# Kernel tuning notes

Hardware: AMD Instinct MI355X
Metric: run time of the kernel (lower is better)

Reference implementation:

```python
import jax, jax.numpy as jnp
import numpy as np

N = 50000   # nodes
E = 800000  # edges (before self-loops)


def _gcn_conv(X, W, b, src, dst, dinv, n):
    # PyG GCNConv: out[i] = sum_j norm_ij * (X W)[j] + b, norm_ij = d_i^-1/2 d_j^-1/2
    h = X @ W                                   # [N, d_out]
    norm = dinv[src] * dinv[dst]                # [E+N]
    msg = h[src] * norm[:, None]                # gather + scale
    return jax.ops.segment_sum(msg, dst, num_segments=n) + b


def setup_inputs() -> dict:
    key = jax.random.key(0)
    k1, k2, k3, k4 = jax.random.split(key, 4)
    X = jax.random.normal(k1, (N, 128), dtype=jnp.float32)
    edge_index = jax.random.randint(k2, (2, E), 0, N, dtype=jnp.int64)
    W1 = jax.random.normal(k3, (128, 128), dtype=jnp.float32) * (1.0 / np.sqrt(128))
    b1 = jnp.zeros((128,), jnp.float32)
    W2 = jax.random.normal(k4, (128, 64), dtype=jnp.float32) * (1.0 / np.sqrt(128))
    b2 = jnp.zeros((64,), jnp.float32)
    return {"X": X, "edge_index": edge_index, "W1": W1, "b1": b1, "W2": W2, "b2": b2}


def reference(X, edge_index, W1, b1, W2, b2):
    n = X.shape[0]
    loops = jnp.arange(n, dtype=edge_index.dtype)
    src = jnp.concatenate([edge_index[0], loops])   # A + I
    dst = jnp.concatenate([edge_index[1], loops])
    deg = jax.ops.segment_sum(jnp.ones(src.shape[0], X.dtype), dst, num_segments=n)
    dinv = jnp.where(deg > 0, jax.lax.rsqrt(deg), 0.0)

    h = _gcn_conv(X, W1, b1, src, dst, dinv, n)                     # gcn1
    h = jax.nn.relu(_gcn_conv(h, W1, b1, src, dst, dinv, n))        # gcn1 again (as in source), relu
    # dropout: eval mode (identity)
    logits = _gcn_conv(h, W2, b2, src, dst, dinv, n)                # gcn2
    return jax.nn.log_softmax(logits, axis=1)
```

## Files before the change

kernel.cpp:

```cpp
#include <hip/hip_runtime.h>
#include <hip/hip_fp16.h>
#include <type_traits>

typedef _Float16 f16x8 __attribute__((ext_vector_type(8)));
typedef float    f32x4 __attribute__((ext_vector_type(4)));

__device__ inline unsigned int pack2(float a, float b) {
    __half2 h = __floats2half2_rn(a, b);
    return *(unsigned int*)&h;
}
__device__ inline float2 unpack2(unsigned int u) {
    __half2 h = *(__half2*)&u;
    return __half22float2(h);
}

#define MAXB 8192


__global__ void zero_kernel(int* __restrict__ p, int len) {
    int i = blockIdx.x * blockDim.x + threadIdx.x;
    if (i < len) p[i] = 0;
}

__global__ __launch_bounds__(256) void bucket_scatter_kernel(
    const int* __restrict__ src, const int* __restrict__ dst, int E, int nbuck,
    int* __restrict__ bcursor, unsigned int* __restrict__ staging) {
    __shared__ int hist[256];
    __shared__ int base[256];
    const int t = threadIdx.x;
    const int chunk = (E + gridDim.x - 1) / gridDim.x;
    const int e0 = blockIdx.x * chunk;
    const int e1 = min(E, e0 + chunk);
    for (int i = t; i < nbuck; i += 256) hist[i] = 0;
    __syncthreads();
    for (int e = e0 + t; e < e1; e += 256)
        atomicAdd(&hist[((unsigned)dst[e]) >> 8], 1);
    __syncthreads();
    for (int i = t; i < nbuck; i += 256) {
        int c = hist[i];
        base[i] = (c > 0) ? atomicAdd(&bcursor[i], c) : 0;
        hist[i] = 0;
    }
    __syncthreads();
    for (int e = e0 + t; e < e1; e += 256) {
        int d = dst[e];
        int b = ((unsigned)d) >> 8;
        int off = atomicAdd(&hist[b], 1);
        staging[(size_t)b * MAXB + base[b] + off] =
            (unsigned)src[e] | ((unsigned)(d & 255) << 16);
    }
}

__global__ __launch_bounds__(256) void bucket_hist_kernel(
    const unsigned int* __restrict__ staging, const int* __restrict__ bcursor,
    int n, int* __restrict__ counts, float* __restrict__ dinv) {
    __shared__ int hist[256];
    const int b = blockIdx.x, t = threadIdx.x;
    hist[t] = 0;
    __syncthreads();
    const int cnt = bcursor[b];
    const unsigned int* rec = staging + (size_t)b * MAXB;
    for (int i = t; i < cnt; i += 256) atomicAdd(&hist[(rec[i] >> 16) & 255], 1);
    __syncthreads();
    int node = (b << 8) + t;
    if (node < n) {
        int c = hist[t];
        counts[node] = c;
        dinv[node]   = rsqrtf(1.0f + (float)c);
    }
}

__global__ __launch_bounds__(256) void scan_small_kernel(const int* __restrict__ in,
                                                         int* __restrict__ out, int nb) {
    __shared__ int s[256];
    int t = threadIdx.x;
    int v = (t < nb) ? in[t] : 0;
    s[t] = v;
    __syncthreads();
    for (int off = 1; off < 256; off <<= 1) {
        int u = (t >= off) ? s[t - off] : 0;
        __syncthreads();
        s[t] += u;
        __syncthreads();
    }
    if (t < nb) out[t] = s[t] - v;
}

__global__ __launch_bounds__(256) void scan_write_kernel(const int* __restrict__ counts,
                                                         const int* __restrict__ blockoff, int n,
                                                         int* __restrict__ rowptr) {
    __shared__ int s[256];
    int t = threadIdx.x;
    int i = blockIdx.x * 256 + t;
    int v = (i < n) ? counts[i] : 0;
    s[t] = v;
    __syncthreads();
    for (int off = 1; off < 256; off <<= 1) {
        int u = (t >= off) ? s[t - off] : 0;
        __syncthreads();
        s[t] += u;
        __syncthreads();
    }
    int excl = blockoff[blockIdx.x] + s[t] - v;
    if (i < n) {
        rowptr[i] = excl;
        if (i == n - 1) rowptr[n] = excl + v;
    }
}

__global__ __launch_bounds__(256) void bucket_place_kernel(
    const unsigned int* __restrict__ staging, const int* __restrict__ bcursor,
    const int* __restrict__ rowptr, int n, unsigned short* __restrict__ edges) {
    __shared__ int lcur[256];
    const int b = blockIdx.x, t = threadIdx.x;
    int node = (b << 8) + t;
    lcur[t] = rowptr[min(node, n)];
    __syncthreads();
    const int cnt = bcursor[b];
    const unsigned int* rec = staging + (size_t)b * MAXB;
    for (int i = t; i < cnt; i += 256) {
        unsigned r = rec[i];
        int dl = (r >> 16) & 255;
        int p  = atomicAdd(&lcur[dl], 1);
        edges[p] = (unsigned short)(r & 0xffffu);
    }
}

template <int DOUT, typename TIN>
__global__ __launch_bounds__(256) void gemm_mfma(const TIN* __restrict__ A,
                                                 const float* __restrict__ W,
                                                 const float* __restrict__ dinv,
                                                 __half* __restrict__ C, int n) {
    constexpr int NF = DOUT / 16;
    __shared__ __align__(16) unsigned char wlds[DOUT * 256];

    const int t = threadIdx.x;
    for (int p = t; p < 64 * DOUT; p += 256) {
        int nn = p % DOUT;
        int k  = (p / DOUT) * 2;
        float w0 = W[(size_t)k * DOUT + nn];
        float w1 = W[(size_t)(k + 1) * DOUT + nn];
        int byte = (nn * 256 + k * 2) ^ ((nn & 7) << 4);
        *(unsigned int*)(wlds + byte) = pack2(w0, w1);
    }
    __syncthreads();

    const int w  = t >> 6;
    const int l  = t & 63;
    const int m  = (blockIdx.x * 4 + w) * 16 + (l & 15);
    const int kq = l >> 4;
    const bool valid = (m < n);

    f32x4 acc[NF];
#pragma unroll
    for (int i = 0; i < NF; ++i) acc[i] = (f32x4){0.f, 0.f, 0.f, 0.f};

#pragma unroll
    for (int ks = 0; ks < 4; ++ks) {
        const int k0 = ks * 32 + kq * 8;
        f16x8 af = {0, 0, 0, 0, 0, 0, 0, 0};
        if (valid) {
            if constexpr (std::is_same<TIN, float>::value) {
                const float4 x0 = *(const float4*)&A[(size_t)m * 128 + k0];
                const float4 x1 = *(const float4*)&A[(size_t)m * 128 + k0 + 4];
                af[0] = (_Float16)x0.x; af[1] = (_Float16)x0.y;
                af[2] = (_Float16)x0.z; af[3] = (_Float16)x0.w;
                af[4] = (_Float16)x1.x; af[5] = (_Float16)x1.y;
                af[6] = (_Float16)x1.z; af[7] = (_Float16)x1.w;
            } else {
                af = *(const f16x8*)&A[(size_t)m * 128 + k0];
            }
        }
#pragma unroll
        for (int nf = 0; nf < NF; ++nf) {
            int nn = nf * 16 + (l & 15);
            int byte = (nn * 256 + k0 * 2) ^ ((nn & 7) << 4);
            f16x8 bf = *(const f16x8*)(wlds + byte);
            acc[nf] = __builtin_amdgcn_mfma_f32_16x16x32_f16(bf, af, acc[nf], 0, 0, 0);
        }
    }

    if (valid) {
        const float di = dinv[m];
#pragma unroll
        for (int nf = 0; nf < NF; ++nf) {
            uint2 o;
            o.x = pack2(di * acc[nf][0], di * acc[nf][1]);
            o.y = pack2(di * acc[nf][2], di * acc[nf][3]);
            *(uint2*)&C[(size_t)m * DOUT + nf * 16 + kq * 4] = o;
        }
    }
}

template <int DOUT, bool RELU, bool LSM, typename TOUT>
__global__ __launch_bounds__(256) void agg_kernel(const __half* __restrict__ H,
                                                  const int* __restrict__ rowptr,
                                                  const unsigned short* __restrict__ edges,
                                                  const float* __restrict__ dinv,
                                                  const float* __restrict__ bias,
                                                  TOUT* __restrict__ out, int n) {
    constexpr int LPR = DOUT / 8;
    constexpr int RPB = 256 / LPR;
    const int row  = blockIdx.x * RPB + threadIdx.x / LPR;
    const int lane = threadIdx.x % LPR;
    if (row >= n) return;

    const uint4* Hv = (const uint4*)H;

    float a[8];
    {
        uint4 h = Hv[(size_t)row * LPR + lane];
        float2 f;
        f = unpack2(h.x); a[0] = f.x; a[1] = f.y;
        f = unpack2(h.y); a[2] = f.x; a[3] = f.y;
        f = unpack2(h.z); a[4] = f.x; a[5] = f.y;
        f = unpack2(h.w); a[6] = f.x; a[7] = f.y;
    }
    auto accum = [&](uint4 h) {
        float2 f;
        f = unpack2(h.x); a[0] += f.x; a[1] += f.y;
        f = unpack2(h.y); a[2] += f.x; a[3] += f.y;
        f = unpack2(h.z); a[4] += f.x; a[5] += f.y;
        f = unpack2(h.w); a[6] += f.x; a[7] += f.y;
    };

    int j        = rowptr[row];
    const int je = rowptr[row + 1];
    for (; j + 3 < je; j += 4) {
        int s0 = edges[j];
        int s1 = edges[j + 1];
        int s2 = edges[j + 2];
        int s3 = edges[j + 3];
        uint4 h0 = Hv[(size_t)s0 * LPR + lane];
        uint4 h1 = Hv[(size_t)s1 * LPR + lane];
        uint4 h2 = Hv[(size_t)s2 * LPR + lane];
        uint4 h3 = Hv[(size_t)s3 * LPR + lane];
        accum(h0); accum(h1); accum(h2); accum(h3);
    }
    for (; j < je; ++j) accum(Hv[(size_t)edges[j] * LPR + lane]);

    const float di = dinv[row];
    const float4 b0 = ((const float4*)bias)[lane * 2];
    const float4 b1 = ((const float4*)bias)[lane * 2 + 1];
    a[0] = b0.x + di * a[0]; a[1] = b0.y + di * a[1];
    a[2] = b0.z + di * a[2]; a[3] = b0.w + di * a[3];
    a[4] = b1.x + di * a[4]; a[5] = b1.y + di * a[5];
    a[6] = b1.z + di * a[6]; a[7] = b1.w + di * a[7];

    if (RELU) {
#pragma unroll
        for (int i = 0; i < 8; ++i) a[i] = fmaxf(a[i], 0.f);
    }

    if constexpr (LSM) {
        float m8 = a[0];
#pragma unroll
        for (int i = 1; i < 8; ++i) m8 = fmaxf(m8, a[i]);
#pragma unroll
        for (int off = 1; off < LPR; off <<= 1) m8 = fmaxf(m8, __shfl_xor(m8, off, LPR));
        float s = 0.f;
#pragma unroll
        for (int i = 0; i < 8; ++i) s += expf(a[i] - m8);
#pragma unroll
        for (int off = 1; off < LPR; off <<= 1) s += __shfl_xor(s, off, LPR);
        float ls = m8 + logf(s);
        float* op = (float*)out + (size_t)row * DOUT + lane * 8;
        *(float4*)op       = make_float4(a[0] - ls, a[1] - ls, a[2] - ls, a[3] - ls);
        *(float4*)(op + 4) = make_float4(a[4] - ls, a[5] - ls, a[6] - ls, a[7] - ls);
    } else {
        uint4 o;
        o.x = pack2(a[0], a[1]);
        o.y = pack2(a[2], a[3]);
        o.z = pack2(a[4], a[5]);
        o.w = pack2(a[6], a[7]);
        *(uint4*)&((__half*)out)[(size_t)row * DOUT + lane * 8] = o;
    }
}


extern "C" void kernel_launch(void* const* d_in, const int* in_sizes, int n_in,
                              void* d_out, int out_size, void* d_ws, size_t ws_size,
                              hipStream_t stream) {
    const float* X  = (const float*)d_in[0];
    const int*   ei = (const int*)d_in[1];
    const float* W1 = (const float*)d_in[2];
    const float* b1 = (const float*)d_in[3];
    const float* W2 = (const float*)d_in[4];
    const float* b2 = (const float*)d_in[5];

    const int n = in_sizes[0] / 128;
    const int E = in_sizes[1] / 2;
    const int* src = ei;
    const int* dst = ei + E;
    const int nbuck = (n + 255) >> 8;

    char* ws = (char*)d_ws;
    size_t off = 0;
    auto alloc = [&](size_t bytes) -> void* {
        void* p = ws + off;
        off = (off + bytes + 255) & ~(size_t)255;
        return p;
    };
    int*            bcursor = (int*)  alloc((size_t)nbuck * 4);
    float*          dinv    = (float*)alloc((size_t)n * 4);
    int*            counts  = (int*)  alloc((size_t)n * 4);
    int*            rowptr  = (int*)  alloc((size_t)(n + 1) * 4);
    int*            bexcl   = (int*)  alloc((size_t)nbuck * 4);
    unsigned int*   staging = (unsigned int*)alloc((size_t)nbuck * MAXB * 4);
    unsigned short* edges   = (unsigned short*)alloc((size_t)E * 2);
    __half*         P       = (__half*)alloc((size_t)n * 128 * 2);
    __half*         Q       = (__half*)alloc((size_t)n * 128 * 2);

    const int nb = (n + 255) / 256;

    zero_kernel<<<1, 256, 0, stream>>>(bcursor, nbuck);
    bucket_scatter_kernel<<<392, 256, 0, stream>>>(src, dst, E, nbuck, bcursor, staging);
    bucket_hist_kernel<<<nbuck, 256, 0, stream>>>(staging, bcursor, n, counts, dinv);
    scan_small_kernel<<<1, 256, 0, stream>>>(bcursor, bexcl, nbuck);
    scan_write_kernel<<<nb, 256, 0, stream>>>(counts, bexcl, n, rowptr);
    bucket_place_kernel<<<nbuck, 256, 0, stream>>>(staging, bcursor, rowptr, n, edges);

    const int gb   = (n + 63) / 64;
    const int ab16 = (n + 15) / 16;
    const int ab32 = (n + 31) / 32;

    gemm_mfma<128, float><<<gb, 256, 0, stream>>>(X, W1, dinv, P, n);
    agg_kernel<128, false, false, __half><<<ab16, 256, 0, stream>>>(
        P, rowptr, edges, dinv, b1, Q, n);

    gemm_mfma<128, __half><<<gb, 256, 0, stream>>>(Q, W1, dinv, P, n);
    agg_kernel<128, true, false, __half><<<ab16, 256, 0, stream>>>(
        P, rowptr, edges, dinv, b1, Q, n);

    gemm_mfma<64, __half><<<gb, 256, 0, stream>>>(Q, W2, dinv, P, n);
    agg_kernel<64, false, true, float><<<ab32, 256, 0, stream>>>(
        P, rowptr, edges, dinv, b2, (float*)d_out, n);
}
```

Measured before the change: 172.5 us.

## Shard 128-wide features into column slabs and pin aggregation slabs per XCC

```diff
diff --git a/kernel.cpp b/kernel.cpp
--- a/kernel.cpp
+++ b/kernel.cpp
@@ -70,11 +70,24 @@
     }
 }
 
-__global__ __launch_bounds__(256) void scan_small_kernel(const int* __restrict__ in,
-                                                         int* __restrict__ out, int nb) {
+__global__ __launch_bounds__(256) void scan_write_kernel(const int* __restrict__ counts,
+                                                         const int* __restrict__ bcursor,
+                                                         int nbuck, int n,
+                                                         int* __restrict__ rowptr) {
+    __shared__ int sb[256];
     __shared__ int s[256];
     int t = threadIdx.x;
-    int v = (t < nb) ? in[t] : 0;
+    sb[t] = (t < nbuck) ? bcursor[t] : 0;
+    __syncthreads();
+    for (int off = 1; off < 256; off <<= 1) {
+        int u = (t >= off) ? sb[t - off] : 0;
+        __syncthreads();
+        sb[t] += u;
+        __syncthreads();
+    }
+    const int blockoff = (blockIdx.x == 0) ? 0 : sb[blockIdx.x - 1];
+    int i = blockIdx.x * 256 + t;
+    int v = (i < n) ? counts[i] : 0;
     s[t] = v;
     __syncthreads();
     for (int off = 1; off < 256; off <<= 1) {
@@ -83,25 +96,7 @@
         s[t] += u;
         __syncthreads();
     }
-    if (t < nb) out[t] = s[t] - v;
-}
-
-__global__ __launch_bounds__(256) void scan_write_kernel(const int* __restrict__ counts,
-                                                         const int* __restrict__ blockoff, int n,
-                                                         int* __restrict__ rowptr) {
-    __shared__ int s[256];
-    int t = threadIdx.x;
-    int i = blockIdx.x * 256 + t;
-    int v = (i < n) ? counts[i] : 0;
-    s[t] = v;
-    __syncthreads();
-    for (int off = 1; off < 256; off <<= 1) {
-        int u = (t >= off) ? s[t - off] : 0;
-        __syncthreads();
-        s[t] += u;
-        __syncthreads();
-    }
-    int excl = blockoff[blockIdx.x] + s[t] - v;
+    int excl = blockoff + s[t] - v;
     if (i < n) {
         rowptr[i] = excl;
         if (i == n - 1) rowptr[n] = excl + v;
@@ -126,7 +121,7 @@
     }
 }
 
-template <int DOUT, typename TIN>
+template <int DOUT, typename TIN, bool OUTQ>
 __global__ __launch_bounds__(256) void gemm_mfma(const TIN* __restrict__ A,
                                                  const float* __restrict__ W,
                                                  const float* __restrict__ dinv,
@@ -168,7 +163,7 @@
                 af[4] = (_Float16)x1.x; af[5] = (_Float16)x1.y;
                 af[6] = (_Float16)x1.z; af[7] = (_Float16)x1.w;
             } else {
-                af = *(const f16x8*)&A[(size_t)m * 128 + k0];
+                af = *(const f16x8*)&A[((size_t)ks * n + m) * 32 + kq * 8];
             }
         }
 #pragma unroll
@@ -187,21 +182,109 @@
             uint2 o;
             o.x = pack2(di * acc[nf][0], di * acc[nf][1]);
             o.y = pack2(di * acc[nf][2], di * acc[nf][3]);
-            *(uint2*)&C[(size_t)m * DOUT + nf * 16 + kq * 4] = o;
+            if constexpr (OUTQ)
+                *(uint2*)&C[((size_t)(nf >> 1) * n + m) * 32 + (nf & 1) * 16 + kq * 4] = o;
+            else
+                *(uint2*)&C[(size_t)m * DOUT + nf * 16 + kq * 4] = o;
         }
     }
 }
 
-template <int DOUT, bool RELU, bool LSM, typename TOUT>
-__global__ __launch_bounds__(256) void agg_kernel(const __half* __restrict__ H,
-                                                  const int* __restrict__ rowptr,
-                                                  const unsigned short* __restrict__ edges,
-                                                  const float* __restrict__ dinv,
-                                                  const float* __restrict__ bias,
-                                                  TOUT* __restrict__ out, int n) {
-    constexpr int LPR = DOUT / 8;
-    constexpr int RPB = 256 / LPR;
-    const int row  = blockIdx.x * RPB + threadIdx.x / LPR;
+template <bool RELU>
+__global__ __launch_bounds__(256) void agg_shard_kernel(
+    const __half* __restrict__ H, const int* __restrict__ rowptr,
+    const unsigned short* __restrict__ edges, const float* __restrict__ dinv,
+    const float* __restrict__ bias, __half* __restrict__ out,
+    int* __restrict__ qhead, int rgq, int n) {
+    __shared__ int sitem, sq;
+    const int t = threadIdx.x;
+    if (t == 0) {
+        unsigned xcc = 0;
+        asm volatile("s_getreg_b32 %0, hwreg(HW_REG_XCC_ID, 0, 4)" : "=s"(xcc));
+        int q = (int)((xcc & 7u) >> 1);
+        int item = atomicAdd(&qhead[q * 32], 1);
+        if (item >= rgq) {
+            item = -1;
+            for (int dq = 1; dq < 4; ++dq) {
+                int q2 = (q + dq) & 3;
+                int it2 = atomicAdd(&qhead[q2 * 32], 1);
+                if (it2 < rgq) { q = q2; item = it2; break; }
+            }
+        }
+        sitem = item;
+        sq = q;
+    }
+    __syncthreads();
+    const int item = sitem;
+    if (item < 0) return;
+    const int q = sq;
+
+    const uint4* Hv = (const uint4*)(H + (size_t)q * n * 32);
+    const int fl = t & 3;
+    const float4 b0 = *(const float4*)&bias[q * 32 + fl * 8];
+    const float4 b1 = *(const float4*)&bias[q * 32 + fl * 8 + 4];
+
+    for (int c = 0; c < 4; ++c) {
+        const int row = item * 256 + c * 64 + (t >> 2);
+        if (row < n) {
+            float a[8];
+            {
+                uint4 h = Hv[(size_t)row * 4 + fl];
+                float2 f;
+                f = unpack2(h.x); a[0] = f.x; a[1] = f.y;
+                f = unpack2(h.y); a[2] = f.x; a[3] = f.y;
+                f = unpack2(h.z); a[4] = f.x; a[5] = f.y;
+                f = unpack2(h.w); a[6] = f.x; a[7] = f.y;
+            }
+            auto accum = [&](uint4 h) {
+                float2 f;
+                f = unpack2(h.x); a[0] += f.x; a[1] += f.y;
+                f = unpack2(h.y); a[2] += f.x; a[3] += f.y;
+                f = unpack2(h.z); a[4] += f.x; a[5] += f.y;
+                f = unpack2(h.w); a[6] += f.x; a[7] += f.y;
+            };
+            int j        = rowptr[row];
+            const int je = rowptr[row + 1];
+            for (; j + 3 < je; j += 4) {
+                int s0 = edges[j];
+                int s1 = edges[j + 1];
+                int s2 = edges[j + 2];
+                int s3 = edges[j + 3];
+                uint4 h0 = Hv[(size_t)s0 * 4 + fl];
+                uint4 h1 = Hv[(size_t)s1 * 4 + fl];
+                uint4 h2 = Hv[(size_t)s2 * 4 + fl];
+                uint4 h3 = Hv[(size_t)s3 * 4 + fl];
+                accum(h0); accum(h1); accum(h2); accum(h3);
+            }
+            for (; j < je; ++j) accum(Hv[(size_t)edges[j] * 4 + fl]);
+
+            const float di = dinv[row];
+            a[0] = b0.x + di * a[0]; a[1] = b0.y + di * a[1];
+            a[2] = b0.z + di * a[2]; a[3] = b0.w + di * a[3];
+            a[4] = b1.x + di * a[4]; a[5] = b1.y + di * a[5];
+            a[6] = b1.z + di * a[6]; a[7] = b1.w + di * a[7];
+            if (RELU) {
+#pragma unroll
+                for (int i = 0; i < 8; ++i) a[i] = fmaxf(a[i], 0.f);
+            }
+            uint4 o;
+            o.x = pack2(a[0], a[1]);
+            o.y = pack2(a[2], a[3]);
+            o.z = pack2(a[4], a[5]);
+            o.w = pack2(a[6], a[7]);
+            *(uint4*)&out[((size_t)q * n + row) * 32 + fl * 8] = o;
+        }
+    }
+}
+
+__global__ __launch_bounds__(256) void agg_lsm_kernel(const __half* __restrict__ H,
+                                                      const int* __restrict__ rowptr,
+                                                      const unsigned short* __restrict__ edges,
+                                                      const float* __restrict__ dinv,
+                                                      const float* __restrict__ bias,
+                                                      float* __restrict__ out, int n) {
+    constexpr int LPR = 8;
+    const int row  = blockIdx.x * 32 + threadIdx.x / LPR;
     const int lane = threadIdx.x % LPR;
     if (row >= n) return;
 
@@ -223,7 +306,6 @@
         f = unpack2(h.z); a[4] += f.x; a[5] += f.y;
         f = unpack2(h.w); a[6] += f.x; a[7] += f.y;
     };
-
     int j        = rowptr[row];
     const int je = rowptr[row + 1];
     for (; j + 3 < je; j += 4) {
@@ -247,34 +329,20 @@
     a[4] = b1.x + di * a[4]; a[5] = b1.y + di * a[5];
     a[6] = b1.z + di * a[6]; a[7] = b1.w + di * a[7];
 
-    if (RELU) {
-#pragma unroll
-        for (int i = 0; i < 8; ++i) a[i] = fmaxf(a[i], 0.f);
-    }
-
-    if constexpr (LSM) {
-        float m8 = a[0];
-#pragma unroll
-        for (int i = 1; i < 8; ++i) m8 = fmaxf(m8, a[i]);
-#pragma unroll
-        for (int off = 1; off < LPR; off <<= 1) m8 = fmaxf(m8, __shfl_xor(m8, off, LPR));
-        float s = 0.f;
-#pragma unroll
-        for (int i = 0; i < 8; ++i) s += expf(a[i] - m8);
-#pragma unroll
-        for (int off = 1; off < LPR; off <<= 1) s += __shfl_xor(s, off, LPR);
-        float ls = m8 + logf(s);
-        float* op = (float*)out + (size_t)row * DOUT + lane * 8;
-        *(float4*)op       = make_float4(a[0] - ls, a[1] - ls, a[2] - ls, a[3] - ls);
-        *(float4*)(op + 4) = make_float4(a[4] - ls, a[5] - ls, a[6] - ls, a[7] - ls);
-    } else {
-        uint4 o;
-        o.x = pack2(a[0], a[1]);
-        o.y = pack2(a[2], a[3]);
-        o.z = pack2(a[4], a[5]);
-        o.w = pack2(a[6], a[7]);
-        *(uint4*)&((__half*)out)[(size_t)row * DOUT + lane * 8] = o;
-    }
+    float m8 = a[0];
+#pragma unroll
+    for (int i = 1; i < 8; ++i) m8 = fmaxf(m8, a[i]);
+#pragma unroll
+    for (int off = 1; off < LPR; off <<= 1) m8 = fmaxf(m8, __shfl_xor(m8, off, LPR));
+    float s = 0.f;
+#pragma unroll
+    for (int i = 0; i < 8; ++i) s += expf(a[i] - m8);
+#pragma unroll
+    for (int off = 1; off < LPR; off <<= 1) s += __shfl_xor(s, off, LPR);
+    float ls = m8 + logf(s);
+    float* op = out + (size_t)row * 64 + lane * 8;
+    *(float4*)op       = make_float4(a[0] - ls, a[1] - ls, a[2] - ls, a[3] - ls);
+    *(float4*)(op + 4) = make_float4(a[4] - ls, a[5] - ls, a[6] - ls, a[7] - ls);
 }
 
 
@@ -301,11 +369,14 @@
         off = (off + bytes + 255) & ~(size_t)255;
         return p;
     };
-    int*            bcursor = (int*)  alloc((size_t)nbuck * 4);
+    const int zlen = nbuck + 256;
+    int*            zbuf    = (int*)  alloc((size_t)zlen * 4);
+    int*            bcursor = zbuf;
+    int*            qh1     = zbuf + nbuck;
+    int*            qh2     = zbuf + nbuck + 128;
     float*          dinv    = (float*)alloc((size_t)n * 4);
     int*            counts  = (int*)  alloc((size_t)n * 4);
     int*            rowptr  = (int*)  alloc((size_t)(n + 1) * 4);
-    int*            bexcl   = (int*)  alloc((size_t)nbuck * 4);
     unsigned int*   staging = (unsigned int*)alloc((size_t)nbuck * MAXB * 4);
     unsigned short* edges   = (unsigned short*)alloc((size_t)E * 2);
     __half*         P       = (__half*)alloc((size_t)n * 128 * 2);
@@ -313,26 +384,23 @@
 
     const int nb = (n + 255) / 256;
 
-    zero_kernel<<<1, 256, 0, stream>>>(bcursor, nbuck);
+    zero_kernel<<<(zlen + 255) / 256, 256, 0, stream>>>(zbuf, zlen);
     bucket_scatter_kernel<<<392, 256, 0, stream>>>(src, dst, E, nbuck, bcursor, staging);
     bucket_hist_kernel<<<nbuck, 256, 0, stream>>>(staging, bcursor, n, counts, dinv);
-    scan_small_kernel<<<1, 256, 0, stream>>>(bcursor, bexcl, nbuck);
-    scan_write_kernel<<<nb, 256, 0, stream>>>(counts, bexcl, n, rowptr);
+    scan_write_kernel<<<nb, 256, 0, stream>>>(counts, bcursor, nbuck, n, rowptr);
     bucket_place_kernel<<<nbuck, 256, 0, stream>>>(staging, bcursor, rowptr, n, edges);
 
     const int gb   = (n + 63) / 64;
-    const int ab16 = (n + 15) / 16;
+    const int rgq  = (n + 255) / 256;
+    const int sgrid = 8 * rgq;
     const int ab32 = (n + 31) / 32;
 
-    gemm_mfma<128, float><<<gb, 256, 0, stream>>>(X, W1, dinv, P, n);
-    agg_kernel<128, false, false, __half><<<ab16, 256, 0, stream>>>(
-        P, rowptr, edges, dinv, b1, Q, n);
-
-    gemm_mfma<128, __half><<<gb, 256, 0, stream>>>(Q, W1, dinv, P, n);
-    agg_kernel<128, true, false, __half><<<ab16, 256, 0, stream>>>(
-        P, rowptr, edges, dinv, b1, Q, n);
-
-    gemm_mfma<64, __half><<<gb, 256, 0, stream>>>(Q, W2, dinv, P, n);
-    agg_kernel<64, false, true, float><<<ab32, 256, 0, stream>>>(
-        P, rowptr, edges, dinv, b2, (float*)d_out, n);
-}
+    gemm_mfma<128, float, true><<<gb, 256, 0, stream>>>(X, W1, dinv, P, n);
+    agg_shard_kernel<false><<<sgrid, 256, 0, stream>>>(P, rowptr, edges, dinv, b1, Q, qh1, rgq, n);
+
+    gemm_mfma<128, __half, true><<<gb, 256, 0, stream>>>(Q, W1, dinv, P, n);
+    agg_shard_kernel<true><<<sgrid, 256, 0, stream>>>(P, rowptr, edges, dinv, b1, Q, qh2, rgq, n);
+
+    gemm_mfma<64, __half, false><<<gb, 256, 0, stream>>>(Q, W2, dinv, P, n);
+    agg_lsm_kernel<<<ab32, 256, 0, stream>>>(P, rowptr, edges, dinv, b2, (float*)d_out, n);
+}
```

After: 212.7 us. +23.3%, slower.

## Fuse graph preprocessing kernels into one persistent kernel with grid barriers

Applied to the files above, without the earlier changes.

```diff
diff --git a/kernel.cpp b/kernel.cpp
--- a/kernel.cpp
+++ b/kernel.cpp
@@ -15,114 +15,102 @@
 }
 
 #define MAXB 8192
-
-
-__global__ void zero_kernel(int* __restrict__ p, int len) {
-    int i = blockIdx.x * blockDim.x + threadIdx.x;
-    if (i < len) p[i] = 0;
-}
-
-__global__ __launch_bounds__(256) void bucket_scatter_kernel(
-    const int* __restrict__ src, const int* __restrict__ dst, int E, int nbuck,
-    int* __restrict__ bcursor, unsigned int* __restrict__ staging) {
-    __shared__ int hist[256];
-    __shared__ int base[256];
-    const int t = threadIdx.x;
-    const int chunk = (E + gridDim.x - 1) / gridDim.x;
-    const int e0 = blockIdx.x * chunk;
-    const int e1 = min(E, e0 + chunk);
-    for (int i = t; i < nbuck; i += 256) hist[i] = 0;
+#define PREP_BLOCKS 384
+
+__device__ inline void grid_barrier(int* ctr, int nblocks) {
     __syncthreads();
-    for (int e = e0 + t; e < e1; e += 256)
-        atomicAdd(&hist[((unsigned)dst[e]) >> 8], 1);
+    if (threadIdx.x == 0) {
+        __threadfence();
+        __hip_atomic_fetch_add(ctr, 1, __ATOMIC_ACQ_REL, __HIP_MEMORY_SCOPE_AGENT);
+        while (__hip_atomic_load(ctr, __ATOMIC_ACQUIRE, __HIP_MEMORY_SCOPE_AGENT) < nblocks) {
+            __builtin_amdgcn_s_sleep(2);
+        }
+        __threadfence();
+    }
     __syncthreads();
-    for (int i = t; i < nbuck; i += 256) {
-        int c = hist[i];
-        base[i] = (c > 0) ? atomicAdd(&bcursor[i], c) : 0;
-        hist[i] = 0;
-    }
-    __syncthreads();
-    for (int e = e0 + t; e < e1; e += 256) {
-        int d = dst[e];
-        int b = ((unsigned)d) >> 8;
-        int off = atomicAdd(&hist[b], 1);
-        staging[(size_t)b * MAXB + base[b] + off] =
-            (unsigned)src[e] | ((unsigned)(d & 255) << 16);
-    }
-}
-
-__global__ __launch_bounds__(256) void bucket_hist_kernel(
-    const unsigned int* __restrict__ staging, const int* __restrict__ bcursor,
-    int n, int* __restrict__ counts, float* __restrict__ dinv) {
-    __shared__ int hist[256];
-    const int b = blockIdx.x, t = threadIdx.x;
-    hist[t] = 0;
-    __syncthreads();
-    const int cnt = bcursor[b];
-    const unsigned int* rec = staging + (size_t)b * MAXB;
-    for (int i = t; i < cnt; i += 256) atomicAdd(&hist[(rec[i] >> 16) & 255], 1);
-    __syncthreads();
-    int node = (b << 8) + t;
-    if (node < n) {
-        int c = hist[t];
-        counts[node] = c;
-        dinv[node]   = rsqrtf(1.0f + (float)c);
-    }
-}
-
-__global__ __launch_bounds__(256) void scan_small_kernel(const int* __restrict__ in,
-                                                         int* __restrict__ out, int nb) {
-    __shared__ int s[256];
-    int t = threadIdx.x;
-    int v = (t < nb) ? in[t] : 0;
-    s[t] = v;
-    __syncthreads();
-    for (int off = 1; off < 256; off <<= 1) {
-        int u = (t >= off) ? s[t - off] : 0;
-        __syncthreads();
-        s[t] += u;
-        __syncthreads();
-    }
-    if (t < nb) out[t] = s[t] - v;
-}
-
-__global__ __launch_bounds__(256) void scan_write_kernel(const int* __restrict__ counts,
-                                                         const int* __restrict__ blockoff, int n,
-                                                         int* __restrict__ rowptr) {
-    __shared__ int s[256];
-    int t = threadIdx.x;
-    int i = blockIdx.x * 256 + t;
-    int v = (i < n) ? counts[i] : 0;
-    s[t] = v;
-    __syncthreads();
-    for (int off = 1; off < 256; off <<= 1) {
-        int u = (t >= off) ? s[t - off] : 0;
-        __syncthreads();
-        s[t] += u;
-        __syncthreads();
-    }
-    int excl = blockoff[blockIdx.x] + s[t] - v;
-    if (i < n) {
-        rowptr[i] = excl;
-        if (i == n - 1) rowptr[n] = excl + v;
-    }
-}
-
-__global__ __launch_bounds__(256) void bucket_place_kernel(
-    const unsigned int* __restrict__ staging, const int* __restrict__ bcursor,
-    const int* __restrict__ rowptr, int n, unsigned short* __restrict__ edges) {
-    __shared__ int lcur[256];
-    const int b = blockIdx.x, t = threadIdx.x;
-    int node = (b << 8) + t;
-    lcur[t] = rowptr[min(node, n)];
-    __syncthreads();
-    const int cnt = bcursor[b];
-    const unsigned int* rec = staging + (size_t)b * MAXB;
-    for (int i = t; i < cnt; i += 256) {
-        unsigned r = rec[i];
-        int dl = (r >> 16) & 255;
-        int p  = atomicAdd(&lcur[dl], 1);
-        edges[p] = (unsigned short)(r & 0xffffu);
+}
+
+__global__ __launch_bounds__(256) void prep_kernel(
+    const int* __restrict__ src, const int* __restrict__ dst, int E, int n, int nbuck,
+    int* __restrict__ bar, int* __restrict__ bcursor,
+    unsigned int* __restrict__ staging, int* __restrict__ rowptr,
+    float* __restrict__ dinv, unsigned short* __restrict__ edges) {
+    __shared__ int A0[256];
+    __shared__ int A1[256];
+    __shared__ int A2[256];
+    const int t   = threadIdx.x;
+    const int bid = blockIdx.x;
+
+    {
+        const int chunk = (E + PREP_BLOCKS - 1) / PREP_BLOCKS;
+        const int e0 = bid * chunk;
+        const int e1 = min(E, e0 + chunk);
+        A0[t] = 0;
+        __syncthreads();
+        for (int e = e0 + t; e < e1; e += 256)
+            atomicAdd(&A0[((unsigned)dst[e]) >> 8], 1);
+        __syncthreads();
+        {
+            int c = A0[t];
+            A1[t] = (c > 0) ? atomicAdd(&bcursor[t], c) : 0;
+            A0[t] = 0;
+        }
+        __syncthreads();
+        for (int e = e0 + t; e < e1; e += 256) {
+            int d = dst[e];
+            int b = ((unsigned)d) >> 8;
+            int off = atomicAdd(&A0[b], 1);
+            staging[(size_t)b * MAXB + A1[b] + off] =
+                (unsigned)src[e] | ((unsigned)(d & 255) << 16);
+        }
+    }
+    grid_barrier(&bar[0], PREP_BLOCKS);
+
+    if (bid < nbuck) {
+        A0[t] = 0;
+        A1[t] = (t < nbuck) ? bcursor[t] : 0;
+        __syncthreads();
+        const int cnt = bcursor[bid];
+        const unsigned int* rec = staging + (size_t)bid * MAXB;
+        for (int i = t; i < cnt; i += 256) atomicAdd(&A0[(rec[i] >> 16) & 255], 1);
+        __syncthreads();
+        for (int off = 1; off < 256; off <<= 1) {
+            int u = (t >= off) ? A1[t - off] : 0;
+            __syncthreads();
+            A1[t] += u;
+            __syncthreads();
+        }
+        const int bexcl = (bid == 0) ? 0 : A1[bid - 1];
+        const int v = A0[t];
+        A2[t] = v;
+        __syncthreads();
+        for (int off = 1; off < 256; off <<= 1) {
+            int u = (t >= off) ? A2[t - off] : 0;
+            __syncthreads();
+            A2[t] += u;
+            __syncthreads();
+        }
+        const int node = (bid << 8) + t;
+        if (node < n) {
+            rowptr[node] = bexcl + A2[t] - v;
+            dinv[node]   = rsqrtf(1.0f + (float)v);
+        }
+        if (bid == 0 && t == 0) rowptr[n] = E;
+    }
+    grid_barrier(&bar[1], PREP_BLOCKS);
+
+    if (bid < nbuck) {
+        const int node = (bid << 8) + t;
+        A0[t] = rowptr[min(node, n)];
+        __syncthreads();
+        const int cnt = bcursor[bid];
+        const unsigned int* rec = staging + (size_t)bid * MAXB;
+        for (int i = t; i < cnt; i += 256) {
+            unsigned r = rec[i];
+            int dl = (r >> 16) & 255;
+            int p  = atomicAdd(&A0[dl], 1);
+            edges[p] = (unsigned short)(r & 0xffffu);
+        }
     }
 }
 
@@ -301,24 +289,20 @@
         off = (off + bytes + 255) & ~(size_t)255;
         return p;
     };
-    int*            bcursor = (int*)  alloc((size_t)nbuck * 4);
+    const int zlen = 8 + nbuck;
+    int*            zbuf    = (int*)  alloc((size_t)zlen * 4);
+    int*            bar     = zbuf;
+    int*            bcursor = zbuf + 8;
     float*          dinv    = (float*)alloc((size_t)n * 4);
-    int*            counts  = (int*)  alloc((size_t)n * 4);
     int*            rowptr  = (int*)  alloc((size_t)(n + 1) * 4);
-    int*            bexcl   = (int*)  alloc((size_t)nbuck * 4);
     unsigned int*   staging = (unsigned int*)alloc((size_t)nbuck * MAXB * 4);
     unsigned short* edges   = (unsigned short*)alloc((size_t)E * 2);
     __half*         P       = (__half*)alloc((size_t)n * 128 * 2);
     __half*         Q       = (__half*)alloc((size_t)n * 128 * 2);
 
-    const int nb = (n + 255) / 256;
-
-    zero_kernel<<<1, 256, 0, stream>>>(bcursor, nbuck);
-    bucket_scatter_kernel<<<392, 256, 0, stream>>>(src, dst, E, nbuck, bcursor, staging);
-    bucket_hist_kernel<<<nbuck, 256, 0, stream>>>(staging, bcursor, n, counts, dinv);
-    scan_small_kernel<<<1, 256, 0, stream>>>(bcursor, bexcl, nbuck);
-    scan_write_kernel<<<nb, 256, 0, stream>>>(counts, bexcl, n, rowptr);
-    bucket_place_kernel<<<nbuck, 256, 0, stream>>>(staging, bcursor, rowptr, n, edges);
+    hipMemsetAsync(zbuf, 0, (size_t)zlen * 4, stream);
+    prep_kernel<<<PREP_BLOCKS, 256, 0, stream>>>(src, dst, E, n, nbuck,
+                                                 bar, bcursor, staging, rowptr, dinv, edges);
 
     const int gb   = (n + 63) / 64;
     const int ab16 = (n + 15) / 16;
```

New measurement: 320.4 us. 85.8% more time.

## Fuse histogram and two scans into one kernel; aggregate two rows per group

Applied to the files above, without the earlier changes.

```diff
diff --git a/kernel.cpp b/kernel.cpp
--- a/kernel.cpp
+++ b/kernel.cpp
@@ -51,61 +51,42 @@
     }
 }
 
-__global__ __launch_bounds__(256) void bucket_hist_kernel(
+__global__ __launch_bounds__(256) void hist_rowptr_kernel(
     const unsigned int* __restrict__ staging, const int* __restrict__ bcursor,
-    int n, int* __restrict__ counts, float* __restrict__ dinv) {
-    __shared__ int hist[256];
+    int nbuck, int n, int E, int* __restrict__ rowptr, float* __restrict__ dinv) {
+    __shared__ int A0[256];
+    __shared__ int A1[256];
+    __shared__ int A2[256];
     const int b = blockIdx.x, t = threadIdx.x;
-    hist[t] = 0;
+    A0[t] = 0;
+    A1[t] = (t < nbuck) ? bcursor[t] : 0;
     __syncthreads();
     const int cnt = bcursor[b];
     const unsigned int* rec = staging + (size_t)b * MAXB;
-    for (int i = t; i < cnt; i += 256) atomicAdd(&hist[(rec[i] >> 16) & 255], 1);
-    __syncthreads();
-    int node = (b << 8) + t;
+    for (int i = t; i < cnt; i += 256) atomicAdd(&A0[(rec[i] >> 16) & 255], 1);
+    __syncthreads();
+    for (int off = 1; off < 256; off <<= 1) {
+        int u = (t >= off) ? A1[t - off] : 0;
+        __syncthreads();
+        A1[t] += u;
+        __syncthreads();
+    }
+    const int bexcl = (b == 0) ? 0 : A1[b - 1];
+    const int v = A0[t];
+    A2[t] = v;
+    __syncthreads();
+    for (int off = 1; off < 256; off <<= 1) {
+        int u = (t >= off) ? A2[t - off] : 0;
+        __syncthreads();
+        A2[t] += u;
+        __syncthreads();
+    }
+    const int node = (b << 8) + t;
     if (node < n) {
-        int c = hist[t];
-        counts[node] = c;
-        dinv[node]   = rsqrtf(1.0f + (float)c);
-    }
-}
-
-__global__ __launch_bounds__(256) void scan_small_kernel(const int* __restrict__ in,
-                                                         int* __restrict__ out, int nb) {
-    __shared__ int s[256];
-    int t = threadIdx.x;
-    int v = (t < nb) ? in[t] : 0;
-    s[t] = v;
-    __syncthreads();
-    for (int off = 1; off < 256; off <<= 1) {
-        int u = (t >= off) ? s[t - off] : 0;
-        __syncthreads();
-        s[t] += u;
-        __syncthreads();
-    }
-    if (t < nb) out[t] = s[t] - v;
-}
-
-__global__ __launch_bounds__(256) void scan_write_kernel(const int* __restrict__ counts,
-                                                         const int* __restrict__ blockoff, int n,
-                                                         int* __restrict__ rowptr) {
-    __shared__ int s[256];
-    int t = threadIdx.x;
-    int i = blockIdx.x * 256 + t;
-    int v = (i < n) ? counts[i] : 0;
-    s[t] = v;
-    __syncthreads();
-    for (int off = 1; off < 256; off <<= 1) {
-        int u = (t >= off) ? s[t - off] : 0;
-        __syncthreads();
-        s[t] += u;
-        __syncthreads();
-    }
-    int excl = blockoff[blockIdx.x] + s[t] - v;
-    if (i < n) {
-        rowptr[i] = excl;
-        if (i == n - 1) rowptr[n] = excl + v;
-    }
+        rowptr[node] = bexcl + A2[t] - v;
+        dinv[node]   = rsqrtf(1.0f + (float)v);
+    }
+    if (b == 0 && t == 0) rowptr[n] = E;
 }
 
 __global__ __launch_bounds__(256) void bucket_place_kernel(
@@ -200,23 +181,25 @@
                                                   const float* __restrict__ bias,
                                                   TOUT* __restrict__ out, int n) {
     constexpr int LPR = DOUT / 8;
-    constexpr int RPB = 256 / LPR;
-    const int row  = blockIdx.x * RPB + threadIdx.x / LPR;
+    constexpr int GPB = 256 / LPR;
+    const int grp  = threadIdx.x / LPR;
     const int lane = threadIdx.x % LPR;
-    if (row >= n) return;
+    const int row0 = (blockIdx.x * GPB + grp) * 2;
+    const int row1 = row0 + 1;
+    if (row0 >= n) return;
+    const bool has1 = (row1 < n);
 
     const uint4* Hv = (const uint4*)H;
 
-    float a[8];
-    {
-        uint4 h = Hv[(size_t)row * LPR + lane];
+    float a0[8], a1[8];
+    auto ld = [&](float* a, uint4 h) {
         float2 f;
         f = unpack2(h.x); a[0] = f.x; a[1] = f.y;
         f = unpack2(h.y); a[2] = f.x; a[3] = f.y;
         f = unpack2(h.z); a[4] = f.x; a[5] = f.y;
         f = unpack2(h.w); a[6] = f.x; a[7] = f.y;
-    }
-    auto accum = [&](uint4 h) {
+    };
+    auto acc = [&](float* a, uint4 h) {
         float2 f;
         f = unpack2(h.x); a[0] += f.x; a[1] += f.y;
         f = unpack2(h.y); a[2] += f.x; a[3] += f.y;
@@ -224,57 +207,90 @@
         f = unpack2(h.w); a[6] += f.x; a[7] += f.y;
     };
 
-    int j        = rowptr[row];
-    const int je = rowptr[row + 1];
-    for (; j + 3 < je; j += 4) {
-        int s0 = edges[j];
-        int s1 = edges[j + 1];
-        int s2 = edges[j + 2];
-        int s3 = edges[j + 3];
+    ld(a0, Hv[(size_t)row0 * LPR + lane]);
+    if (has1) ld(a1, Hv[(size_t)row1 * LPR + lane]);
+    else {
+#pragma unroll
+        for (int i = 0; i < 8; ++i) a1[i] = 0.f;
+    }
+
+    int j0 = rowptr[row0];
+    const int je0 = rowptr[row0 + 1];
+    int j1 = has1 ? rowptr[row1] : 0;
+    const int je1 = has1 ? rowptr[row1 + 1] : 0;
+
+    while (j0 + 3 < je0 && j1 + 3 < je1) {
+        int s00 = edges[j0], s01 = edges[j0 + 1], s02 = edges[j0 + 2], s03 = edges[j0 + 3];
+        int s10 = edges[j1], s11 = edges[j1 + 1], s12 = edges[j1 + 2], s13 = edges[j1 + 3];
+        uint4 h00 = Hv[(size_t)s00 * LPR + lane];
+        uint4 h01 = Hv[(size_t)s01 * LPR + lane];
+        uint4 h02 = Hv[(size_t)s02 * LPR + lane];
+        uint4 h03 = Hv[(size_t)s03 * LPR + lane];
+        uint4 h10 = Hv[(size_t)s10 * LPR + lane];
+        uint4 h11 = Hv[(size_t)s11 * LPR + lane];
+        uint4 h12 = Hv[(size_t)s12 * LPR + lane];
+        uint4 h13 = Hv[(size_t)s13 * LPR + lane];
+        acc(a0, h00); acc(a0, h01); acc(a0, h02); acc(a0, h03);
+        acc(a1, h10); acc(a1, h11); acc(a1, h12); acc(a1, h13);
+        j0 += 4; j1 += 4;
+    }
+    for (; j0 + 3 < je0; j0 += 4) {
+        int s0 = edges[j0], s1 = edges[j0 + 1], s2 = edges[j0 + 2], s3 = edges[j0 + 3];
         uint4 h0 = Hv[(size_t)s0 * LPR + lane];
         uint4 h1 = Hv[(size_t)s1 * LPR + lane];
         uint4 h2 = Hv[(size_t)s2 * LPR + lane];
         uint4 h3 = Hv[(size_t)s3 * LPR + lane];
-        accum(h0); accum(h1); accum(h2); accum(h3);
-    }
-    for (; j < je; ++j) accum(Hv[(size_t)edges[j] * LPR + lane]);
-
-    const float di = dinv[row];
+        acc(a0, h0); acc(a0, h1); acc(a0, h2); acc(a0, h3);
+    }
+    for (; j0 < je0; ++j0) acc(a0, Hv[(size_t)edges[j0] * LPR + lane]);
+    for (; j1 + 3 < je1; j1 += 4) {
+        int s0 = edges[j1], s1 = edges[j1 + 1], s2 = edges[j1 + 2], s3 = edges[j1 + 3];
+        uint4 h0 = Hv[(size_t)s0 * LPR + lane];
+        uint4 h1 = Hv[(size_t)s1 * LPR + lane];
+        uint4 h2 = Hv[(size_t)s2 * LPR + lane];
+        uint4 h3 = Hv[(size_t)s3 * LPR + lane];
+        acc(a1, h0); acc(a1, h1); acc(a1, h2); acc(a1, h3);
+    }
+    for (; j1 < je1; ++j1) acc(a1, Hv[(size_t)edges[j1] * LPR + lane]);
+
     const float4 b0 = ((const float4*)bias)[lane * 2];
     const float4 b1 = ((const float4*)bias)[lane * 2 + 1];
-    a[0] = b0.x + di * a[0]; a[1] = b0.y + di * a[1];
-    a[2] = b0.z + di * a[2]; a[3] = b0.w + di * a[3];
-    a[4] = b1.x + di * a[4]; a[5] = b1.y + di * a[5];
-    a[6] = b1.z + di * a[6]; a[7] = b1.w + di * a[7];
-
-    if (RELU) {
-#pragma unroll
-        for (int i = 0; i < 8; ++i) a[i] = fmaxf(a[i], 0.f);
-    }
-
-    if constexpr (LSM) {
-        float m8 = a[0];
-#pragma unroll
-        for (int i = 1; i < 8; ++i) m8 = fmaxf(m8, a[i]);
-#pragma unroll
-        for (int off = 1; off < LPR; off <<= 1) m8 = fmaxf(m8, __shfl_xor(m8, off, LPR));
-        float s = 0.f;
-#pragma unroll
-        for (int i = 0; i < 8; ++i) s += expf(a[i] - m8);
-#pragma unroll
-        for (int off = 1; off < LPR; off <<= 1) s += __shfl_xor(s, off, LPR);
-        float ls = m8 + logf(s);
-        float* op = (float*)out + (size_t)row * DOUT + lane * 8;
-        *(float4*)op       = make_float4(a[0] - ls, a[1] - ls, a[2] - ls, a[3] - ls);
-        *(float4*)(op + 4) = make_float4(a[4] - ls, a[5] - ls, a[6] - ls, a[7] - ls);
-    } else {
-        uint4 o;
-        o.x = pack2(a[0], a[1]);
-        o.y = pack2(a[2], a[3]);
-        o.z = pack2(a[4], a[5]);
-        o.w = pack2(a[6], a[7]);
-        *(uint4*)&((__half*)out)[(size_t)row * DOUT + lane * 8] = o;
-    }
+    auto finish = [&](float* a, int row) {
+        const float di = dinv[row];
+        a[0] = b0.x + di * a[0]; a[1] = b0.y + di * a[1];
+        a[2] = b0.z + di * a[2]; a[3] = b0.w + di * a[3];
+        a[4] = b1.x + di * a[4]; a[5] = b1.y + di * a[5];
+        a[6] = b1.z + di * a[6]; a[7] = b1.w + di * a[7];
+        if (RELU) {
+#pragma unroll
+            for (int i = 0; i < 8; ++i) a[i] = fmaxf(a[i], 0.f);
+        }
+        if constexpr (LSM) {
+            float m8 = a[0];
+#pragma unroll
+            for (int i = 1; i < 8; ++i) m8 = fmaxf(m8, a[i]);
+#pragma unroll
+            for (int off = 1; off < LPR; off <<= 1) m8 = fmaxf(m8, __shfl_xor(m8, off, LPR));
+            float s = 0.f;
+#pragma unroll
+            for (int i = 0; i < 8; ++i) s += expf(a[i] - m8);
+#pragma unroll
+            for (int off = 1; off < LPR; off <<= 1) s += __shfl_xor(s, off, LPR);
+            float ls = m8 + logf(s);
+            float* op = (float*)out + (size_t)row * DOUT + lane * 8;
+            *(float4*)op       = make_float4(a[0] - ls, a[1] - ls, a[2] - ls, a[3] - ls);
+            *(float4*)(op + 4) = make_float4(a[4] - ls, a[5] - ls, a[6] - ls, a[7] - ls);
+        } else {
+            uint4 o;
+            o.x = pack2(a[0], a[1]);
+            o.y = pack2(a[2], a[3]);
+            o.z = pack2(a[4], a[5]);
+            o.w = pack2(a[6], a[7]);
+            *(uint4*)&((__half*)out)[(size_t)row * DOUT + lane * 8] = o;
+        }
+    };
+    finish(a0, row0);
+    if (has1) finish(a1, row1);
 }
 
 
@@ -303,26 +319,20 @@
     };
     int*            bcursor = (int*)  alloc((size_t)nbuck * 4);
     float*          dinv    = (float*)alloc((size_t)n * 4);
-    int*            counts  = (int*)  alloc((size_t)n * 4);
     int*            rowptr  = (int*)  alloc((size_t)(n + 1) * 4);
-    int*            bexcl   = (int*)  alloc((size_t)nbuck * 4);
     unsigned int*   staging = (unsigned int*)alloc((size_t)nbuck * MAXB * 4);
     unsigned short* edges   = (unsigned short*)alloc((size_t)E * 2);
     __half*         P       = (__half*)alloc((size_t)n * 128 * 2);
     __half*         Q       = (__half*)alloc((size_t)n * 128 * 2);
 
-    const int nb = (n + 255) / 256;
-
     zero_kernel<<<1, 256, 0, stream>>>(bcursor, nbuck);
     bucket_scatter_kernel<<<392, 256, 0, stream>>>(src, dst, E, nbuck, bcursor, staging);
-    bucket_hist_kernel<<<nbuck, 256, 0, stream>>>(staging, bcursor, n, counts, dinv);
-    scan_small_kernel<<<1, 256, 0, stream>>>(bcursor, bexcl, nbuck);
-    scan_write_kernel<<<nb, 256, 0, stream>>>(counts, bexcl, n, rowptr);
+    hist_rowptr_kernel<<<nbuck, 256, 0, stream>>>(staging, bcursor, nbuck, n, E, rowptr, dinv);
     bucket_place_kernel<<<nbuck, 256, 0, stream>>>(staging, bcursor, rowptr, n, edges);
 
     const int gb   = (n + 63) / 64;
-    const int ab16 = (n + 15) / 16;
-    const int ab32 = (n + 31) / 32;
+    const int ab16 = (n + 31) / 32;
+    const int ab32 = (n + 63) / 64;
 
     gemm_mfma<128, float><<<gb, 256, 0, stream>>>(X, W1, dinv, P, n);
     agg_kernel<128, false, false, __half><<<ab16, 256, 0, stream>>>(
```

Result: slower. 191.5 us (+11.0%).
